# Kernel tuning notes

Hardware: AMD Instinct MI355X
Metric: run time of the kernel (lower is better)

Reference implementation:

```python
import jax, jax.numpy as jnp
import numpy as np

B = 32768          # rays
N = 512            # gaussians
NSH = 4            # -> m = 2*NSH+1 = 9 SH coeffs
H = 512.0
W = 512.0
S_MIN = 1.0 / 30.0       # 1 / n_gaussian_max_pixels
S_MAX = 1.0 / 0.75       # 1 / n_gaussian_min_pixels
MU_BORDER = 1.05
PI_APPROX = 3.1416       # matches the literal in the torch source


def setup_inputs() -> dict:
    key = jax.random.key(0)
    ks = jax.random.split(key, 6)
    # pixel coordinates in [0, W) x [0, H)
    x = jax.random.uniform(ks[0], (B, 2), jnp.float32) * jnp.array([W, H], jnp.float32)
    rgbsh = jax.random.uniform(ks[1], (N, 2 * NSH + 1, 3), jnp.float32)
    opacity = jax.random.uniform(ks[2], (N,), jnp.float32)
    mu = jax.random.uniform(ks[3], (N, 2), jnp.float32) * 2.0 - 1.0
    scale = jax.random.uniform(ks[4], (N, 2), jnp.float32)
    angle = jax.random.uniform(ks[5], (N,), jnp.float32) * 2.0 - 1.0
    return {"x": x, "rgbsh": rgbsh, "opacity": opacity,
            "mu": mu, "scale": scale, "angle": angle}


def _forward(x, rgbsh, opacity, mu, scale, angle):
    wh = jnp.array([W, H], x.dtype)                      # (2,)
    xnorm = x / wh * 2.0 - 1.0                           # (B,2) in [-1,1]
    gmu = jnp.tanh(mu) * MU_BORDER                       # (N,2)
    S = jnp.clip(scale, 0.0, 1.0) * (S_MAX - S_MIN) + S_MIN  # (N,2) inverse radii

    # pixel-space offset ray->gaussian: (x - mu)/2 * (w,h)
    vec = (xnorm[:, None, :] - gmu[None, :, :]) * (wh * 0.5)   # (B,N,2)

    # validity mask (computed under no_grad in torch): |S * vec| < 5
    dist = jnp.linalg.norm(vec * S[None], axis=-1)             # (B,N)
    valid = jax.lax.stop_gradient(dist < 5.0)

    # per-gaussian rotation matrices
    alpha = jnp.tanh(angle) * PI_APPROX                        # (N,)
    c, s = jnp.cos(alpha), jnp.sin(alpha)
    R = jnp.stack([jnp.stack([c, -s], -1),
                   jnp.stack([s,  c], -1)], axis=-2)           # (N,2,2)

    # Mahalanobis-like squared distance: || R @ diag(S) @ vec ||^2
    svec = vec * S[None]                                       # (B,N,2)
    rot = jnp.einsum('nij,bnj->bni', R, svec)                  # (B,N,2)
    d2 = jnp.sum(rot * rot, axis=-1)                           # (B,N)

    # view angle in the gaussian frame
    vnorm = vec / (1e-10 + jnp.linalg.norm(vec, axis=-1, keepdims=True))
    vrot = jnp.einsum('nij,bnj->bni', R, vnorm)                # (B,N,2)
    theta = jnp.arctan2(vrot[..., 0], vrot[..., 1])            # (B,N)

    # 2D SH basis: [1, sin(t), cos(t), sin(2t), cos(2t), ...]
    basis = [jnp.ones_like(theta)]
    for i in range(NSH):
        basis.append(jnp.sin(theta * (i + 1)))
        basis.append(jnp.cos(theta * (i + 1)))
    basis = jnp.stack(basis, axis=-1)                          # (B,N,M)

    rgb = jax.nn.sigmoid(jnp.einsum('bnm,nmc->bnc', basis, rgbsh))  # (B,N,3)
    wgt = jnp.where(valid,
                    jnp.exp(-d2) * jax.nn.sigmoid(opacity)[None, :],
                    jnp.zeros((), x.dtype))                    # (B,N)

    # accumulate_along_rays: per-ray weighted sum over gaussians
    return jnp.einsum('bn,bnc->bc', wgt, rgb)                  # (B,3)


def reference(x, rgbsh, opacity, mu, scale, angle):
    return _forward(x, rgbsh, opacity, mu, scale, angle)
```

## Files before the change

kernel.cpp:

```cpp
#include <hip/hip_runtime.h>

#define BDIM 512
#define NW   8
#define RPB  64
#define NG   512
#define GPW  64
#define QCAP 256


__global__ void pre_kernel(const float* __restrict__ rgbsh,
                           const float* __restrict__ opacity,
                           const float* __restrict__ mu,
                           const float* __restrict__ scale,
                           const float* __restrict__ angle,
                           float4* __restrict__ wsA,
                           float*  __restrict__ wsH,
                           int N)
{
    int n = blockIdx.x * blockDim.x + threadIdx.x;
    if (n >= N) return;
    const float S_MIN = 1.0f / 30.0f;
    const float S_MAX = 1.0f / 0.75f;
    float gmx = tanhf(mu[2 * n + 0]) * 1.05f;
    float gmy = tanhf(mu[2 * n + 1]) * 1.05f;
    float Sx = fminf(fmaxf(scale[2 * n + 0], 0.0f), 1.0f) * (S_MAX - S_MIN) + S_MIN;
    float Sy = fminf(fmaxf(scale[2 * n + 1], 0.0f), 1.0f) * (S_MAX - S_MIN) + S_MIN;
    float ax = 256.0f * Sx, ay = 256.0f * Sy;
    wsA[n] = make_float4(ax, ay, -gmx * ax, -gmy * ay);
    float a = tanhf(angle[n]) * 3.1416f;
    float sa, ca;
    sincosf(a, &sa, &ca);
    float* hp = wsH + ((size_t)n << 5);
    hp[0] = ca;
    hp[1] = sa;
    hp[2] = 1.0f / (1.0f + expf(-opacity[n]));
    hp[3] = 1.0f / Sx;
    hp[4] = 1.0f / Sy;
    #pragma unroll
    for (int q = 0; q < 27; ++q) hp[5 + q] = rgbsh[n * 27 + q];
}

__global__ __launch_bounds__(BDIM, 4) void splat_kernel(
    const float*  __restrict__ x,
    const float4* __restrict__ wsA,
    const float*  __restrict__ wsH,
    float* __restrict__ out,
    int B)
{
    __shared__ float acc[NW][RPB * 3];
    __shared__ unsigned short queue[NW][QCAP];
    const int tid  = threadIdx.x;
    const int lane = tid & 63;
    const int w = __builtin_amdgcn_readfirstlane(tid >> 6);

    const int   gid = w * GPW + lane;
    const float4 pa = wsA[gid];

    const int b  = blockIdx.x * RPB + lane;
    const int bb = (b < B) ? b : (B - 1);
    float2 p2 = *(const float2*)(x + 2 * bb);
    const float pnx = p2.x * (1.0f / 256.0f) - 1.0f;
    const float pny = p2.y * (1.0f / 256.0f) - 1.0f;
    const int ipnx = __builtin_bit_cast(int, pnx);
    const int ipny = __builtin_bit_cast(int, pny);

    #pragma unroll
    for (int c = 0; c < 3; ++c) acc[w][lane * 3 + c] = 0.0f;
    __syncthreads();

    int qlen = 0;

    auto flush = [&]() {
        const int qtot = (qlen + 63) & ~63;
        for (int qi = lane; qi < qtot; qi += 64) {
            const bool live = (qi < qlen);
            const int e  = live ? (int)queue[w][qi] : 0;
            const int r  = e >> 6;
            const int gl = e & 63;
            const float qx = __builtin_bit_cast(float,
                __builtin_amdgcn_ds_bpermute(r << 2, ipnx));
            const float qy = __builtin_bit_cast(float,
                __builtin_amdgcn_ds_bpermute(r << 2, ipny));
            const int g = w * GPW + gl;
            const float4 pb = wsA[g];
            const float sx = fmaf(qx, pb.x, pb.z);
            const float sy = fmaf(qy, pb.y, pb.w);
            const float4* hp = (const float4*)(wsH + ((size_t)g << 5));
            const float4 f0 = hp[0], f1 = hp[1], f2 = hp[2], f3 = hp[3];
            const float4 f4 = hp[4], f5 = hp[5], f6 = hp[6], f7 = hp[7];
            const float c = f0.x, s = f0.y, w0 = f0.z, iSx = f0.w, iSy = f1.x;
            float rx = fmaf(c, sx, -s * sy);
            float ry = fmaf(s, sx,  c * sy);
            float d2 = fmaf(rx, rx, ry * ry);
            float vx  = sx * iSx;
            float vy  = sy * iSy;
            float len = sqrtf(fmaf(vx, vx, vy * vy));
            float inv = __builtin_amdgcn_rcpf(1e-10f + len);
            float rvx = fmaf(c, vx, -s * vy);
            float rvy = fmaf(s, vx,  c * vy);
            float s1 = rvx * inv, c1 = rvy * inv;
            float s2 = 2.0f * s1 * c1;
            float c2 = fmaf(c1, c1, -s1 * s1);
            float s3 = fmaf(s2, c1,  c2 * s1);
            float c3 = fmaf(c2, c1, -s2 * s1);
            float s4 = 2.0f * s2 * c2;
            float c4 = fmaf(c2, c2, -s2 * s2);
            float rr = f1.y, gg = f1.z, bb2 = f1.w;
            rr = fmaf(s1, f2.x, rr);  gg = fmaf(s1, f2.y, gg);  bb2 = fmaf(s1, f2.z, bb2);
            rr = fmaf(c1, f2.w, rr);  gg = fmaf(c1, f3.x, gg);  bb2 = fmaf(c1, f3.y, bb2);
            rr = fmaf(s2, f3.z, rr);  gg = fmaf(s2, f3.w, gg);  bb2 = fmaf(s2, f4.x, bb2);
            rr = fmaf(c2, f4.y, rr);  gg = fmaf(c2, f4.z, gg);  bb2 = fmaf(c2, f4.w, bb2);
            rr = fmaf(s3, f5.x, rr);  gg = fmaf(s3, f5.y, gg);  bb2 = fmaf(s3, f5.z, bb2);
            rr = fmaf(c3, f5.w, rr);  gg = fmaf(c3, f6.x, gg);  bb2 = fmaf(c3, f6.y, bb2);
            rr = fmaf(s4, f6.z, rr);  gg = fmaf(s4, f6.w, gg);  bb2 = fmaf(s4, f7.x, bb2);
            rr = fmaf(c4, f7.y, rr);  gg = fmaf(c4, f7.z, gg);  bb2 = fmaf(c4, f7.w, bb2);
            rr  = __builtin_amdgcn_rcpf(1.0f + __expf(-rr));
            gg  = __builtin_amdgcn_rcpf(1.0f + __expf(-gg));
            bb2 = __builtin_amdgcn_rcpf(1.0f + __expf(-bb2));
            float wt = __expf(-d2) * w0;
            if (live) {
                atomicAdd(&acc[w][r * 3 + 0], wt * rr);
                atomicAdd(&acc[w][r * 3 + 1], wt * gg);
                atomicAdd(&acc[w][r * 3 + 2], wt * bb2);
            }
        }
        qlen = 0;
    };

    #pragma unroll
    for (int r = 0; r < RPB; ++r) {
        const float spx = __builtin_bit_cast(float,
            __builtin_amdgcn_readlane(ipnx, r));
        const float spy = __builtin_bit_cast(float,
            __builtin_amdgcn_readlane(ipny, r));
        float sx = fmaf(spx, pa.x, pa.z);
        float sy = fmaf(spy, pa.y, pa.w);
        float t  = fmaf(sx, sx, sy * sy);
        bool  v  = t < 25.0f;
        unsigned long long mask = __ballot(v);
        if (mask) {
            int prefix = __popcll(mask & ((1ull << lane) - 1ull));
            if (v) queue[w][qlen + prefix] = (unsigned short)((r << 6) | lane);
            qlen += __popcll(mask);
            if (qlen > QCAP - 64) flush();
        }
    }
    flush();

    __syncthreads();
    if (tid < RPB * 3) {
        float s = 0.0f;
        #pragma unroll
        for (int w2 = 0; w2 < NW; ++w2)
            s += acc[w2][tid];
        const int idx = blockIdx.x * (RPB * 3) + tid;
        if (idx < 3 * B)
            out[idx] = s;
    }
}

extern "C" void kernel_launch(void* const* d_in, const int* in_sizes, int n_in,
                              void* d_out, int out_size, void* d_ws, size_t ws_size,
                              hipStream_t stream) {
    const float* x       = (const float*)d_in[0];
    const float* rgbsh   = (const float*)d_in[1];
    const float* opacity = (const float*)d_in[2];
    const float* mu      = (const float*)d_in[3];
    const float* scale   = (const float*)d_in[4];
    const float* angle   = (const float*)d_in[5];
    float* out = (float*)d_out;

    const int B = in_sizes[0] / 2;
    const int N = in_sizes[2];

    char* ws = (char*)d_ws;
    float4* wsA = (float4*)(ws);
    float*  wsH = (float*)(ws + (size_t)N * 16);

    pre_kernel<<<(N + 255) / 256, 256, 0, stream>>>(rgbsh, opacity, mu, scale,
                                                    angle, wsA, wsH, N);
    splat_kernel<<<(B + RPB - 1) / RPB, BDIM, 0, stream>>>(x, wsA, wsH, out, B);
}
```

Before: 72.10 us.

## Fuse gaussian preprocessing into splat kernel and stage params in LDS

Removes the separate pre_kernel launch and its workspace round-trip. Each block recomputes per-gaussian transforms (tanh, sincos, sigmoid, inverse scales) for its own 64 gaussians per wave and stores them in shared memory. The flush loop then reads geometry from LDS and SH coefficients directly from the unaligned rgbsh global array. This saves one launch and global traffic, at the cost of redundant transcendental work in every block and scalar unaligned loads in place of float4 loads. The __syncthreads before the loop is also dropped, which relies on each wave touching only its own LDS slice.

After: 69.77 us. -3.2%, faster.

```diff
diff --git a/kernel.cpp b/kernel.cpp
--- a/kernel.cpp
+++ b/kernel.cpp
@@ -3,58 +3,29 @@
 #define BDIM 512
 #define NW   8
 #define RPB  64
-#define NG   512
 #define GPW  64
 #define QCAP 256
+#define PROW 12
 
 
-__global__ void pre_kernel(const float* __restrict__ rgbsh,
-                           const float* __restrict__ opacity,
-                           const float* __restrict__ mu,
-                           const float* __restrict__ scale,
-                           const float* __restrict__ angle,
-                           float4* __restrict__ wsA,
-                           float*  __restrict__ wsH,
-                           int N)
+__global__ __launch_bounds__(BDIM, 4) void splat_kernel(
+    const float* __restrict__ x,
+    const float* __restrict__ rgbsh,
+    const float* __restrict__ opacity,
+    const float* __restrict__ mu,
+    const float* __restrict__ scale,
+    const float* __restrict__ angle,
+    float* __restrict__ out,
+    int B, int N)
 {
-    int n = blockIdx.x * blockDim.x + threadIdx.x;
-    if (n >= N) return;
-    const float S_MIN = 1.0f / 30.0f;
-    const float S_MAX = 1.0f / 0.75f;
-    float gmx = tanhf(mu[2 * n + 0]) * 1.05f;
-    float gmy = tanhf(mu[2 * n + 1]) * 1.05f;
-    float Sx = fminf(fmaxf(scale[2 * n + 0], 0.0f), 1.0f) * (S_MAX - S_MIN) + S_MIN;
-    float Sy = fminf(fmaxf(scale[2 * n + 1], 0.0f), 1.0f) * (S_MAX - S_MIN) + S_MIN;
-    float ax = 256.0f * Sx, ay = 256.0f * Sy;
-    wsA[n] = make_float4(ax, ay, -gmx * ax, -gmy * ay);
-    float a = tanhf(angle[n]) * 3.1416f;
-    float sa, ca;
-    sincosf(a, &sa, &ca);
-    float* hp = wsH + ((size_t)n << 5);
-    hp[0] = ca;
-    hp[1] = sa;
-    hp[2] = 1.0f / (1.0f + expf(-opacity[n]));
-    hp[3] = 1.0f / Sx;
-    hp[4] = 1.0f / Sy;
-    #pragma unroll
-    for (int q = 0; q < 27; ++q) hp[5 + q] = rgbsh[n * 27 + q];
-}
-
-__global__ __launch_bounds__(BDIM, 4) void splat_kernel(
-    const float*  __restrict__ x,
-    const float4* __restrict__ wsA,
-    const float*  __restrict__ wsH,
-    float* __restrict__ out,
-    int B)
-{
+    __shared__ float prm[NW][GPW][PROW];
     __shared__ float acc[NW][RPB * 3];
     __shared__ unsigned short queue[NW][QCAP];
+
     const int tid  = threadIdx.x;
     const int lane = tid & 63;
-    const int w = __builtin_amdgcn_readfirstlane(tid >> 6);
-
-    const int   gid = w * GPW + lane;
-    const float4 pa = wsA[gid];
+    const int w    = __builtin_amdgcn_readfirstlane(tid >> 6);
+    const int gid  = w * GPW + lane;
 
     const int b  = blockIdx.x * RPB + lane;
     const int bb = (b < B) ? b : (B - 1);
@@ -64,9 +35,29 @@
     const int ipnx = __builtin_bit_cast(int, pnx);
     const int ipny = __builtin_bit_cast(int, pny);
 
+    float pax, pay, pbx, pby;
+    {
+        const float S_MIN = 1.0f / 30.0f;
+        const float S_MAX = 1.0f / 0.75f;
+        float2 muv = *(const float2*)(mu + 2 * gid);
+        float2 scv = *(const float2*)(scale + 2 * gid);
+        float gmx = tanhf(muv.x) * 1.05f;
+        float gmy = tanhf(muv.y) * 1.05f;
+        float Sx = fminf(fmaxf(scv.x, 0.0f), 1.0f) * (S_MAX - S_MIN) + S_MIN;
+        float Sy = fminf(fmaxf(scv.y, 0.0f), 1.0f) * (S_MAX - S_MIN) + S_MIN;
+        pax = 256.0f * Sx;  pay = 256.0f * Sy;
+        pbx = -gmx * pax;   pby = -gmy * pay;
+        float a = tanhf(angle[gid]) * 3.1416f;
+        float sa, ca;
+        sincosf(a, &sa, &ca);
+        float w0 = 1.0f / (1.0f + expf(-opacity[gid]));
+        float* pr = &prm[w][lane][0];
+        pr[0] = pax; pr[1] = pay; pr[2] = pbx; pr[3] = pby;
+        pr[4] = ca;  pr[5] = sa;  pr[6] = w0;
+        pr[7] = 1.0f / Sx;  pr[8] = 1.0f / Sy;
+    }
     #pragma unroll
     for (int c = 0; c < 3; ++c) acc[w][lane * 3 + c] = 0.0f;
-    __syncthreads();
 
     int qlen = 0;
 
@@ -81,14 +72,12 @@
                 __builtin_amdgcn_ds_bpermute(r << 2, ipnx));
             const float qy = __builtin_bit_cast(float,
                 __builtin_amdgcn_ds_bpermute(r << 2, ipny));
-            const int g = w * GPW + gl;
-            const float4 pb = wsA[g];
-            const float sx = fmaf(qx, pb.x, pb.z);
-            const float sy = fmaf(qy, pb.y, pb.w);
-            const float4* hp = (const float4*)(wsH + ((size_t)g << 5));
-            const float4 f0 = hp[0], f1 = hp[1], f2 = hp[2], f3 = hp[3];
-            const float4 f4 = hp[4], f5 = hp[5], f6 = hp[6], f7 = hp[7];
-            const float c = f0.x, s = f0.y, w0 = f0.z, iSx = f0.w, iSy = f1.x;
+            const float4 g0 = *(const float4*)&prm[w][gl][0];
+            const float4 g1 = *(const float4*)&prm[w][gl][4];
+            const float iSy = prm[w][gl][8];
+            const float sx = fmaf(qx, g0.x, g0.z);
+            const float sy = fmaf(qy, g0.y, g0.w);
+            const float c = g1.x, s = g1.y, w0 = g1.z, iSx = g1.w;
             float rx = fmaf(c, sx, -s * sy);
             float ry = fmaf(s, sx,  c * sy);
             float d2 = fmaf(rx, rx, ry * ry);
@@ -105,15 +94,16 @@
             float c3 = fmaf(c2, c1, -s2 * s1);
             float s4 = 2.0f * s2 * c2;
             float c4 = fmaf(c2, c2, -s2 * s2);
-            float rr = f1.y, gg = f1.z, bb2 = f1.w;
-            rr = fmaf(s1, f2.x, rr);  gg = fmaf(s1, f2.y, gg);  bb2 = fmaf(s1, f2.z, bb2);
-            rr = fmaf(c1, f2.w, rr);  gg = fmaf(c1, f3.x, gg);  bb2 = fmaf(c1, f3.y, bb2);
-            rr = fmaf(s2, f3.z, rr);  gg = fmaf(s2, f3.w, gg);  bb2 = fmaf(s2, f4.x, bb2);
-            rr = fmaf(c2, f4.y, rr);  gg = fmaf(c2, f4.z, gg);  bb2 = fmaf(c2, f4.w, bb2);
-            rr = fmaf(s3, f5.x, rr);  gg = fmaf(s3, f5.y, gg);  bb2 = fmaf(s3, f5.z, bb2);
-            rr = fmaf(c3, f5.w, rr);  gg = fmaf(c3, f6.x, gg);  bb2 = fmaf(c3, f6.y, bb2);
-            rr = fmaf(s4, f6.z, rr);  gg = fmaf(s4, f6.w, gg);  bb2 = fmaf(s4, f7.x, bb2);
-            rr = fmaf(c4, f7.y, rr);  gg = fmaf(c4, f7.z, gg);  bb2 = fmaf(c4, f7.w, bb2);
+            const float* sh = rgbsh + (size_t)(w * GPW + gl) * 27;
+            float rr = sh[0], gg = sh[1], bb2 = sh[2];
+            rr = fmaf(s1, sh[ 3], rr);  gg = fmaf(s1, sh[ 4], gg);  bb2 = fmaf(s1, sh[ 5], bb2);
+            rr = fmaf(c1, sh[ 6], rr);  gg = fmaf(c1, sh[ 7], gg);  bb2 = fmaf(c1, sh[ 8], bb2);
+            rr = fmaf(s2, sh[ 9], rr);  gg = fmaf(s2, sh[10], gg);  bb2 = fmaf(s2, sh[11], bb2);
+            rr = fmaf(c2, sh[12], rr);  gg = fmaf(c2, sh[13], gg);  bb2 = fmaf(c2, sh[14], bb2);
+            rr = fmaf(s3, sh[15], rr);  gg = fmaf(s3, sh[16], gg);  bb2 = fmaf(s3, sh[17], bb2);
+            rr = fmaf(c3, sh[18], rr);  gg = fmaf(c3, sh[19], gg);  bb2 = fmaf(c3, sh[20], bb2);
+            rr = fmaf(s4, sh[21], rr);  gg = fmaf(s4, sh[22], gg);  bb2 = fmaf(s4, sh[23], bb2);
+            rr = fmaf(c4, sh[24], rr);  gg = fmaf(c4, sh[25], gg);  bb2 = fmaf(c4, sh[26], bb2);
             rr  = __builtin_amdgcn_rcpf(1.0f + __expf(-rr));
             gg  = __builtin_amdgcn_rcpf(1.0f + __expf(-gg));
             bb2 = __builtin_amdgcn_rcpf(1.0f + __expf(-bb2));
@@ -133,8 +123,8 @@
             __builtin_amdgcn_readlane(ipnx, r));
         const float spy = __builtin_bit_cast(float,
             __builtin_amdgcn_readlane(ipny, r));
-        float sx = fmaf(spx, pa.x, pa.z);
-        float sy = fmaf(spy, pa.y, pa.w);
+        float sx = fmaf(spx, pax, pbx);
+        float sy = fmaf(spy, pay, pby);
         float t  = fmaf(sx, sx, sy * sy);
         bool  v  = t < 25.0f;
         unsigned long long mask = __ballot(v);
@@ -173,11 +163,6 @@
     const int B = in_sizes[0] / 2;
     const int N = in_sizes[2];
 
-    char* ws = (char*)d_ws;
-    float4* wsA = (float4*)(ws);
-    float*  wsH = (float*)(ws + (size_t)N * 16);
-
-    pre_kernel<<<(N + 255) / 256, 256, 0, stream>>>(rgbsh, opacity, mu, scale,
-                                                    angle, wsA, wsH, N);
-    splat_kernel<<<(B + RPB - 1) / RPB, BDIM, 0, stream>>>(x, wsA, wsH, out, B);
+    splat_kernel<<<(B + RPB - 1) / RPB, BDIM, 0, stream>>>(
+        x, rgbsh, opacity, mu, scale, angle, out, B, N);
 }
```
